# Performance work log

Hardware: AMD Instinct MI355X
Metric: run time of the kernel (lower is better)

## Reference

```python
import jax, jax.numpy as jnp
import numpy as np

N, D = 8192, 768
EPS = 1e-5  # torch LayerNorm default


def setup_inputs() -> dict:
    key = jax.random.key(0)
    ks = jax.random.split(key, 5)
    q = jax.random.normal(ks[0], (N, D), dtype=jnp.float32)
    k = jax.random.normal(ks[1], (N, D), dtype=jnp.float32)
    v = jax.random.normal(ks[2], (N, D), dtype=jnp.float32)
    ln_w = jnp.ones((D,), dtype=jnp.float32)
    ln_b = jnp.zeros((D,), dtype=jnp.float32)
    W_qkv = jax.random.normal(ks[3], (D, D), dtype=jnp.float32) * 0.02
    W_proj = jax.random.normal(ks[4], (D, D), dtype=jnp.float32) * 0.02
    b_proj = jnp.zeros((D,), dtype=jnp.float32)
    return {"q": q, "k": k, "v": v, "ln_w": ln_w, "ln_b": ln_b,
            "W_qkv": W_qkv, "W_proj": W_proj, "b_proj": b_proj}


def reference(q, k, v, ln_w, ln_b, W_qkv, W_proj, b_proj):
    dim = q.shape[-1]
    scale = dim ** (-0.5)

    def ln(x):
        mu = jnp.mean(x, axis=-1, keepdims=True)
        var = jnp.mean((x - mu) ** 2, axis=-1, keepdims=True)
        return (x - mu) * jax.lax.rsqrt(var + EPS) * ln_w + ln_b

    # shared LayerNorm + shared Linear (toto0, no bias) applied to q, k, v
    qn = ln(q) @ W_qkv.T  # [N, D]
    kn = ln(k) @ W_qkv.T
    vn = ln(v) @ W_qkv.T

    attn = jnp.einsum('qc,kc->qk', qn, kn) * scale  # [N, N]
    attn = jax.nn.softmax(attn, axis=-1)
    out = jnp.einsum('qk,kc->qc', attn, vn)  # [N, D]
    out = out @ W_proj.T + b_proj  # proj0
    return out
```

## Files before the change

kernel.cpp:

```cpp
#include <hip/hip_runtime.h>
#include <hip/hip_bf16.h>
#include <stdint.h>

typedef short bf16x8 __attribute__((ext_vector_type(8)));
typedef float f32x4 __attribute__((ext_vector_type(4)));
typedef unsigned short u16;
typedef u16 u16x8 __attribute__((ext_vector_type(8)));

__device__ __forceinline__ u16 f2bf(float x) {
  __hip_bfloat16 h = __float2bfloat16(x);
  return *reinterpret_cast<u16*>(&h);
}
__device__ __forceinline__ float bf2f(u16 v) {
  unsigned u = (unsigned)v << 16;
  return *reinterpret_cast<float*>(&u);
}

__device__ __forceinline__ void gload_lds16(const void* g, const void* lds_base) {
  __builtin_amdgcn_global_load_lds(
      (const __attribute__((address_space(1))) unsigned int*)(uintptr_t)g,
      (__attribute__((address_space(3))) unsigned int*)(uintptr_t)lds_base,
      16, 0, 0);
}

__global__ __launch_bounds__(256) void ln_cast_kernel(
    const float* __restrict__ q, const float* __restrict__ k, const float* __restrict__ v,
    const float* __restrict__ lw, const float* __restrict__ lb, u16* __restrict__ out) {
  int row = blockIdx.x;
  const float* x;
  if (row < 8192) x = q + (size_t)row * 768;
  else if (row < 16384) x = k + (size_t)(row - 8192) * 768;
  else x = v + (size_t)(row - 16384) * 768;
  int t = threadIdx.x;
  float a0 = x[t], a1 = x[t + 256], a2 = x[t + 512];
  __shared__ float red[4];
  __shared__ float red2[4];
  float s = a0 + a1 + a2;
  for (int o = 32; o; o >>= 1) s += __shfl_down(s, o, 64);
  if ((t & 63) == 0) red[t >> 6] = s;
  __syncthreads();
  float mean = (red[0] + red[1] + red[2] + red[3]) * (1.0f / 768.0f);
  float d0 = a0 - mean, d1 = a1 - mean, d2 = a2 - mean;
  float vs = d0 * d0 + d1 * d1 + d2 * d2;
  for (int o = 32; o; o >>= 1) vs += __shfl_down(vs, o, 64);
  if ((t & 63) == 0) red2[t >> 6] = vs;
  __syncthreads();
  float var = (red2[0] + red2[1] + red2[2] + red2[3]) * (1.0f / 768.0f);
  float rstd = rsqrtf(var + 1e-5f);
  u16* o_ = out + (size_t)row * 768;
  o_[t]       = f2bf(d0 * rstd * lw[t]       + lb[t]);
  o_[t + 256] = f2bf(d1 * rstd * lw[t + 256] + lb[t + 256]);
  o_[t + 512] = f2bf(d2 * rstd * lw[t + 512] + lb[t + 512]);
}

__global__ __launch_bounds__(256) void cast_f32_bf16(const float* __restrict__ in,
                                                     u16* __restrict__ out, int n4) {
  int i = blockIdx.x * 256 + threadIdx.x;
  if (i < n4) {
    float4 vv = ((const float4*)in)[i];
    ushort4 o;
    o.x = f2bf(vv.x); o.y = f2bf(vv.y); o.z = f2bf(vv.z); o.w = f2bf(vv.w);
    ((ushort4*)out)[i] = o;
  }
}

__global__ __launch_bounds__(256) void zero_f32(float* __restrict__ p, int n) {
  int i = blockIdx.x * 256 + threadIdx.x;
  if (i < n) p[i] = 0.0f;
}

__global__ __launch_bounds__(256) void transpose64(const u16* __restrict__ in, u16* __restrict__ out) {
  __shared__ __align__(16) u16 tile[64][72];
  int b = blockIdx.x;
  int tr = b / 12, tc = b % 12;
  int t = threadIdx.x;
  int r = t >> 3;
  int cb = (t & 7) << 3;
#pragma unroll
  for (int i = 0; i < 2; i++) {
    int row = r + i * 32;
    const u16* src = in + (size_t)(tr * 64 + row) * 768 + tc * 64 + cb;
    *(uint4*)&tile[row][cb] = *(const uint4*)src;
  }
  __syncthreads();
#pragma unroll
  for (int i = 0; i < 2; i++) {
    int oc = r + i * 32;
    u16x8 tmp;
#pragma unroll
    for (int j = 0; j < 8; j++) tmp[j] = tile[cb + j][oc];
    u16* dst = out + (size_t)(tc * 64 + oc) * 8192 + tr * 64 + cb;
    *(u16x8*)dst = tmp;
  }
}

__global__ __launch_bounds__(256) void reduce4_scale(
    const u16* __restrict__ p0, const u16* __restrict__ p1,
    const u16* __restrict__ p2, const u16* __restrict__ p3,
    const float* __restrict__ rowsum, u16* __restrict__ out, int n8) {
  int i = blockIdx.x * 256 + threadIdx.x;
  if (i < n8) {
    float inv = 1.0f / rowsum[i / 96];
    u16x8 a = ((const u16x8*)p0)[i];
    u16x8 b = ((const u16x8*)p1)[i];
    u16x8 c = ((const u16x8*)p2)[i];
    u16x8 d = ((const u16x8*)p3)[i];
    u16x8 o;
#pragma unroll
    for (int j = 0; j < 8; j++)
      o[j] = f2bf((bf2f(a[j]) + bf2f(b[j]) + bf2f(c[j]) + bf2f(d[j])) * inv);
    ((u16x8*)out)[i] = o;
  }
}

template <int MODE>
__global__ __launch_bounds__(256, 2) void gemm_bt(
    const u16* __restrict__ A0, const u16* __restrict__ B0,
    void* __restrict__ Cv0, void* __restrict__ Cv1,
    int M, int N, int K, int lda, int ldb, int ldc,
    float scale, const float* __restrict__ bias, float* __restrict__ rowsum,
    size_t cSplitStride) {
  __shared__ __align__(16) u16 sA[128 * 64];
  __shared__ __align__(16) u16 sB[128 * 64];
  const int z = blockIdx.y;
  const u16* A = A0 + (size_t)z * (size_t)K;
  const u16* B = B0 + (size_t)z * (size_t)K;
  u16* Cb = (z < 2) ? ((u16*)Cv0 + (size_t)z * cSplitStride)
                    : ((u16*)Cv1 + (size_t)(z - 2) * cSplitStride);
  const int nTn = N >> 7;
  int nwg = gridDim.x, orig = blockIdx.x;
  int qq = nwg >> 3, rr = nwg & 7;
  int xcd = orig & 7, loc = orig >> 3;
  int wg = (xcd < rr ? xcd * (qq + 1) : rr * (qq + 1) + (xcd - rr) * qq) + loc;
  int tm, tn;
  if (nTn == 64 && (M >> 7) == 64) {
    int sb = wg >> 4, in_ = wg & 15;
    tm = ((sb >> 4) << 2) | (in_ >> 2);
    tn = ((sb & 15) << 2) | (in_ & 3);
  } else {
    tm = wg / nTn; tn = wg % nTn;
  }

  const int t = threadIdx.x, l = t & 63, w = t >> 6;
  const int wr = w >> 1, wc = w & 1;
  const int lr = l & 15, kg = (l >> 4) << 3;

  f32x4 acc[4][4];
#pragma unroll
  for (int m = 0; m < 4; m++)
#pragma unroll
    for (int n = 0; n < 4; n++) acc[m][n] = (f32x4){0.f, 0.f, 0.f, 0.f};

  const size_t rowA0 = (size_t)tm * 128;
  const size_t rowB0 = (size_t)tn * 128;
  const int nk = K >> 6;
  for (int kt = 0; kt < nk; kt++) {
    const int k0 = kt << 6;
#pragma unroll
    for (int i = 0; i < 4; i++) {
      int chunk = i * 256 + t;
      int row = chunk >> 3;
      int col = (chunk & 7) << 3;
      gload_lds16(A + (rowA0 + row) * lda + k0 + col, (const char*)sA + (i * 256 + w * 64) * 16);
      gload_lds16(B + (rowB0 + row) * ldb + k0 + col, (const char*)sB + (i * 256 + w * 64) * 16);
    }
    __syncthreads();
#pragma unroll
    for (int kk = 0; kk < 2; kk++) {
      bf16x8 af[4], bfv[4];
#pragma unroll
      for (int m = 0; m < 4; m++)
        af[m] = *(const bf16x8*)&sA[(wr * 64 + m * 16 + lr) * 64 + kk * 32 + kg];
#pragma unroll
      for (int n = 0; n < 4; n++)
        bfv[n] = *(const bf16x8*)&sB[(wc * 64 + n * 16 + lr) * 64 + kk * 32 + kg];
#pragma unroll
      for (int m = 0; m < 4; m++)
#pragma unroll
        for (int n = 0; n < 4; n++)
          acc[m][n] = __builtin_amdgcn_mfma_f32_16x16x32_bf16(af[m], bfv[n], acc[m][n], 0, 0, 0);
    }
    __syncthreads();
  }
  if (MODE == 1) {
    float rs[4][4];
#pragma unroll
    for (int m = 0; m < 4; m++)
#pragma unroll
      for (int j = 0; j < 4; j++) rs[m][j] = 0.0f;
#pragma unroll
    for (int m = 0; m < 4; m++) {
      int rowb = tm * 128 + wr * 64 + m * 16 + ((l >> 4) << 2);
#pragma unroll
      for (int n = 0; n < 4; n++) {
        int col = tn * 128 + wc * 64 + n * 16 + lr;
#pragma unroll
        for (int j = 0; j < 4; j++) {
          float e = __expf(acc[m][n][j] * scale);
          Cb[(size_t)(rowb + j) * ldc + col] = f2bf(e);
          rs[m][j] += e;
        }
      }
    }
#pragma unroll
    for (int m = 0; m < 4; m++) {
      int rowb = tm * 128 + wr * 64 + m * 16 + ((l >> 4) << 2);
#pragma unroll
      for (int j = 0; j < 4; j++) {
        float r = rs[m][j];
        r += __shfl_xor(r, 1);
        r += __shfl_xor(r, 2);
        r += __shfl_xor(r, 4);
        r += __shfl_xor(r, 8);
        if ((l & 15) == 0) atomicAdd(&rowsum[rowb + j], r);
      }
    }
  } else {
#pragma unroll
    for (int m = 0; m < 4; m++) {
      int row = tm * 128 + wr * 64 + m * 16 + ((l >> 4) << 2);
#pragma unroll
      for (int n = 0; n < 4; n++) {
        int col = tn * 128 + wc * 64 + n * 16 + lr;
#pragma unroll
        for (int j = 0; j < 4; j++) {
          float vl = acc[m][n][j];
          if (MODE == 0) Cb[(size_t)(row + j) * ldc + col] = f2bf(vl * scale);
          else ((float*)Cv0)[(size_t)(row + j) * ldc + col] = vl + bias[col];
        }
      }
    }
  }
}

extern "C" void kernel_launch(void* const* d_in, const int* in_sizes, int n_in,
                              void* d_out, int out_size, void* d_ws, size_t ws_size,
                              hipStream_t stream) {
  const float* q  = (const float*)d_in[0];
  const float* k  = (const float*)d_in[1];
  const float* v  = (const float*)d_in[2];
  const float* lw = (const float*)d_in[3];
  const float* lb = (const float*)d_in[4];
  const float* Wq = (const float*)d_in[5];
  const float* Wp = (const float*)d_in[6];
  const float* bp = (const float*)d_in[7];

  char* ws = (char*)d_ws;
  size_t off = 0;
  auto alloc = [&](size_t b) { size_t o = off; off += (b + 255) & ~(size_t)255; return o; };
  size_t o_ln = alloc((size_t)24576 * 768 * 2);
  size_t o_pj = alloc((size_t)24576 * 768 * 2);
  size_t o_wq = alloc((size_t)768 * 768 * 2);
  size_t o_wp = alloc((size_t)768 * 768 * 2);
  u16* lnbuf = (u16*)(ws + o_ln);
  u16* pj    = (u16*)(ws + o_pj);
  u16* wqb   = (u16*)(ws + o_wq);
  u16* wpb   = (u16*)(ws + o_wp);
  const size_t NS = (size_t)8192 * 768;
  u16* vnT = lnbuf;
  u16* p0  = lnbuf + NS;
  u16* p1  = lnbuf + 2 * NS;
  float* rowsum = (float*)(pj + 2 * NS);
  u16* p2 = (u16*)d_out;
  u16* p3 = p2 + NS;
  size_t fixedEnd = off;
  u16* Sbuf = (u16*)(ws + fixedEnd);

  const float scale = 0.03608439182435161f;

  ln_cast_kernel<<<dim3(24576), dim3(256), 0, stream>>>(q, k, v, lw, lb, lnbuf);
  cast_f32_bf16<<<dim3(576), dim3(256), 0, stream>>>(Wq, wqb, 147456);
  cast_f32_bf16<<<dim3(576), dim3(256), 0, stream>>>(Wp, wpb, 147456);

  gemm_bt<0><<<dim3(1152), dim3(256), 0, stream>>>(lnbuf, wqb, (void*)pj, (void*)pj,
      24576, 768, 768, 768, 768, 768, 1.0f, (const float*)nullptr, (float*)nullptr, 0);

  transpose64<<<dim3(1536), dim3(256), 0, stream>>>(pj + (size_t)16384 * 768, vnT);
  zero_f32<<<dim3(32), dim3(256), 0, stream>>>(rowsum, 8192);

  gemm_bt<1><<<dim3(4096), dim3(256), 0, stream>>>(
      pj, pj + NS, (void*)Sbuf, (void*)Sbuf,
      8192, 8192, 768, 768, 768, 8192, scale, (const float*)nullptr, rowsum, 0);

  gemm_bt<0><<<dim3(384, 4), dim3(256), 0, stream>>>(
      Sbuf, vnT, (void*)p0, (void*)p2,
      8192, 768, 2048, 8192, 8192, 768, 1.0f, (const float*)nullptr, (float*)nullptr, NS);

  reduce4_scale<<<dim3(3072), dim3(256), 0, stream>>>(p0, p1, p2, p3, rowsum, p0, (int)(NS / 8));

  gemm_bt<2><<<dim3(384), dim3(256), 0, stream>>>(p0, wpb, d_out, d_out,
      8192, 768, 768, 768, 768, 768, 1.0f, bp, (float*)nullptr, 0);
}
```

Baseline: 381.4 us.

## Add dedicated 256x256 double-buffered QK^T exp kernel with swizzled LDS

```diff
diff --git a/kernel.cpp b/kernel.cpp
--- a/kernel.cpp
+++ b/kernel.cpp
@@ -22,6 +22,10 @@
       (__attribute__((address_space(3))) unsigned int*)(uintptr_t)lds_base,
       16, 0, 0);
 }
+
+#define BAR() __builtin_amdgcn_s_barrier()
+#define LG0() asm volatile("s_waitcnt lgkmcnt(0)" ::: "memory")
+#define VM0() asm volatile("s_waitcnt vmcnt(0)" ::: "memory")
 
 __global__ __launch_bounds__(256) void ln_cast_kernel(
     const float* __restrict__ q, const float* __restrict__ k, const float* __restrict__ v,
@@ -113,13 +117,129 @@
   }
 }
 
+__global__ __launch_bounds__(512, 2) void qk_exp_256(
+    const u16* __restrict__ A, const u16* __restrict__ B, u16* __restrict__ C,
+    float* __restrict__ rowsum, float scale) {
+  __shared__ __align__(16) u16 sA[2][256 * 64];
+  __shared__ __align__(16) u16 sB[2][256 * 64];
+  int orig = blockIdx.x;
+  int wg = (orig & 7) * 128 + (orig >> 3);
+  int tm = wg >> 5, tn = wg & 31;
+  const int t = threadIdx.x, l = t & 63, w = t >> 6;
+  const int wr = w >> 2, wc = w & 3;
+  const int lr = l & 15, lq = l >> 4;
+  const int colb = lq * 16;
+  const int rswz = (lr & 7) << 4;
+
+  f32x4 acc[8][4];
+#pragma unroll
+  for (int m = 0; m < 8; m++)
+#pragma unroll
+    for (int n = 0; n < 4; n++) acc[m][n] = (f32x4){0.f, 0.f, 0.f, 0.f};
+
+  const size_t rA0 = (size_t)tm * 256, rB0 = (size_t)tn * 256;
+
+  auto SCALL = [&](int bufsel, int T, int idx) {
+    const u16* src = (idx < 4) ? A : B;
+    size_t r0 = (idx < 4) ? rA0 : rB0;
+    u16* dstbase = (idx < 4) ? sA[bufsel] : sB[bufsel];
+    int p = idx & 3, k0 = T << 6;
+    int x = p * 8192 + t * 16;
+    int r = x >> 7;
+    int cb = (x & 127) ^ ((r & 7) << 4);
+    gload_lds16((const char*)(src + (r0 + r) * 768 + k0) + cb,
+                (const char*)dstbase + p * 8192 + w * 1024);
+  };
+  auto LOADA = [&](bf16x8 (&aF)[4], int d, int mh, int kk) {
+#pragma unroll
+    for (int mf = 0; mf < 4; mf++) {
+      int arow = wr * 128 + (mh * 4 + mf) * 16 + lr;
+      int x = arow * 128 + kk * 64 + colb;
+      aF[mf] = *(const bf16x8*)((const char*)sA[d] + (x ^ rswz));
+    }
+  };
+  auto LOADB = [&](bf16x8 (&bF)[4], int d, int kk) {
+#pragma unroll
+    for (int nf = 0; nf < 4; nf++) {
+      int brow = wc * 64 + nf * 16 + lr;
+      int x = brow * 128 + kk * 64 + colb;
+      bF[nf] = *(const bf16x8*)((const char*)sB[d] + (x ^ rswz));
+    }
+  };
+  auto MM = [&](bf16x8 (&aF)[4], bf16x8 (&bF)[4], int mh) {
+    __builtin_amdgcn_s_setprio(1);
+#pragma unroll
+    for (int mf = 0; mf < 4; mf++)
+#pragma unroll
+      for (int nf = 0; nf < 4; nf++)
+        acc[mh * 4 + mf][nf] = __builtin_amdgcn_mfma_f32_16x16x32_bf16(
+            aF[mf], bF[nf], acc[mh * 4 + mf][nf], 0, 0, 0);
+    __builtin_amdgcn_s_setprio(0);
+  };
+
+#pragma unroll
+  for (int idx = 0; idx < 8; idx++) SCALL(0, 0, idx);
+  VM0();
+  BAR();
+
+  for (int T = 0; T < 12; T++) {
+    const int cur = T & 1, nxt = cur ^ 1;
+    const bool pf = (T < 11);
+    bf16x8 aF[4], bF0[4], bF1[4];
+    LOADA(aF, cur, 0, 0); LOADB(bF0, cur, 0);
+    if (pf) { SCALL(nxt, T + 1, 0); SCALL(nxt, T + 1, 1); }
+    BAR(); LG0(); MM(aF, bF0, 0); BAR();
+    LOADA(aF, cur, 1, 0);
+    if (pf) { SCALL(nxt, T + 1, 2); SCALL(nxt, T + 1, 3); }
+    BAR(); LG0(); MM(aF, bF0, 1); BAR();
+    LOADA(aF, cur, 0, 1); LOADB(bF1, cur, 1);
+    if (pf) { SCALL(nxt, T + 1, 4); SCALL(nxt, T + 1, 5); }
+    BAR(); LG0(); MM(aF, bF1, 0); BAR();
+    LOADA(aF, cur, 1, 1);
+    if (pf) { SCALL(nxt, T + 1, 6); SCALL(nxt, T + 1, 7); }
+    BAR(); LG0(); MM(aF, bF1, 1);
+    VM0();
+    BAR();
+  }
+
+  float rs[8][4];
+#pragma unroll
+  for (int m = 0; m < 8; m++)
+#pragma unroll
+    for (int j = 0; j < 4; j++) rs[m][j] = 0.0f;
+  const size_t rowBase = rA0 + (size_t)wr * 128;
+  const int colBase = tn * 256 + wc * 64;
+#pragma unroll
+  for (int mi = 0; mi < 8; mi++) {
+    size_t row0 = rowBase + mi * 16 + lq * 4;
+#pragma unroll
+    for (int nf = 0; nf < 4; nf++) {
+      int col = colBase + nf * 16 + lr;
+#pragma unroll
+      for (int j = 0; j < 4; j++) {
+        float e = __expf(acc[mi][nf][j] * scale);
+        C[(row0 + j) * 8192 + col] = f2bf(e);
+        rs[mi][j] += e;
+      }
+    }
+  }
+#pragma unroll
+  for (int mi = 0; mi < 8; mi++)
+#pragma unroll
+    for (int j = 0; j < 4; j++) {
+      float r = rs[mi][j];
+      r += __shfl_xor(r, 1); r += __shfl_xor(r, 2);
+      r += __shfl_xor(r, 4); r += __shfl_xor(r, 8);
+      if (lr == 0) atomicAdd(&rowsum[rowBase + mi * 16 + lq * 4 + j], r);
+    }
+}
+
 template <int MODE>
 __global__ __launch_bounds__(256, 2) void gemm_bt(
     const u16* __restrict__ A0, const u16* __restrict__ B0,
     void* __restrict__ Cv0, void* __restrict__ Cv1,
     int M, int N, int K, int lda, int ldb, int ldc,
-    float scale, const float* __restrict__ bias, float* __restrict__ rowsum,
-    size_t cSplitStride) {
+    float scale, const float* __restrict__ bias, size_t cSplitStride) {
   __shared__ __align__(16) u16 sA[128 * 64];
   __shared__ __align__(16) u16 sB[128 * 64];
   const int z = blockIdx.y;
@@ -132,14 +252,7 @@
   int qq = nwg >> 3, rr = nwg & 7;
   int xcd = orig & 7, loc = orig >> 3;
   int wg = (xcd < rr ? xcd * (qq + 1) : rr * (qq + 1) + (xcd - rr) * qq) + loc;
-  int tm, tn;
-  if (nTn == 64 && (M >> 7) == 64) {
-    int sb = wg >> 4, in_ = wg & 15;
-    tm = ((sb >> 4) << 2) | (in_ >> 2);
-    tn = ((sb & 15) << 2) | (in_ & 3);
-  } else {
-    tm = wg / nTn; tn = wg % nTn;
-  }
+  int tm = wg / nTn, tn = wg % nTn;
 
   const int t = threadIdx.x, l = t & 63, w = t >> 6;
   const int wr = w >> 1, wc = w & 1;
@@ -182,52 +295,17 @@
     }
     __syncthreads();
   }
-  if (MODE == 1) {
-    float rs[4][4];
-#pragma unroll
-    for (int m = 0; m < 4; m++)
-#pragma unroll
-      for (int j = 0; j < 4; j++) rs[m][j] = 0.0f;
-#pragma unroll
-    for (int m = 0; m < 4; m++) {
-      int rowb = tm * 128 + wr * 64 + m * 16 + ((l >> 4) << 2);
-#pragma unroll
-      for (int n = 0; n < 4; n++) {
-        int col = tn * 128 + wc * 64 + n * 16 + lr;
-#pragma unroll
-        for (int j = 0; j < 4; j++) {
-          float e = __expf(acc[m][n][j] * scale);
-          Cb[(size_t)(rowb + j) * ldc + col] = f2bf(e);
-          rs[m][j] += e;
-        }
-      }
-    }
-#pragma unroll
-    for (int m = 0; m < 4; m++) {
-      int rowb = tm * 128 + wr * 64 + m * 16 + ((l >> 4) << 2);
+#pragma unroll
+  for (int m = 0; m < 4; m++) {
+    int row = tm * 128 + wr * 64 + m * 16 + ((l >> 4) << 2);
+#pragma unroll
+    for (int n = 0; n < 4; n++) {
+      int col = tn * 128 + wc * 64 + n * 16 + lr;
 #pragma unroll
       for (int j = 0; j < 4; j++) {
-        float r = rs[m][j];
-        r += __shfl_xor(r, 1);
-        r += __shfl_xor(r, 2);
-        r += __shfl_xor(r, 4);
-        r += __shfl_xor(r, 8);
-        if ((l & 15) == 0) atomicAdd(&rowsum[rowb + j], r);
-      }
-    }
-  } else {
-#pragma unroll
-    for (int m = 0; m < 4; m++) {
-      int row = tm * 128 + wr * 64 + m * 16 + ((l >> 4) << 2);
-#pragma unroll
-      for (int n = 0; n < 4; n++) {
-        int col = tn * 128 + wc * 64 + n * 16 + lr;
-#pragma unroll
-        for (int j = 0; j < 4; j++) {
-          float vl = acc[m][n][j];
-          if (MODE == 0) Cb[(size_t)(row + j) * ldc + col] = f2bf(vl * scale);
-          else ((float*)Cv0)[(size_t)(row + j) * ldc + col] = vl + bias[col];
-        }
+        float vl = acc[m][n][j];
+        if (MODE == 0) Cb[(size_t)(row + j) * ldc + col] = f2bf(vl * scale);
+        else ((float*)Cv0)[(size_t)(row + j) * ldc + col] = vl + bias[col];
       }
     }
   }
@@ -273,21 +351,19 @@
   cast_f32_bf16<<<dim3(576), dim3(256), 0, stream>>>(Wp, wpb, 147456);
 
   gemm_bt<0><<<dim3(1152), dim3(256), 0, stream>>>(lnbuf, wqb, (void*)pj, (void*)pj,
-      24576, 768, 768, 768, 768, 768, 1.0f, (const float*)nullptr, (float*)nullptr, 0);
+      24576, 768, 768, 768, 768, 768, 1.0f, (const float*)nullptr, 0);
 
   transpose64<<<dim3(1536), dim3(256), 0, stream>>>(pj + (size_t)16384 * 768, vnT);
   zero_f32<<<dim3(32), dim3(256), 0, stream>>>(rowsum, 8192);
 
-  gemm_bt<1><<<dim3(4096), dim3(256), 0, stream>>>(
-      pj, pj + NS, (void*)Sbuf, (void*)Sbuf,
-      8192, 8192, 768, 768, 768, 8192, scale, (const float*)nullptr, rowsum, 0);
+  qk_exp_256<<<dim3(1024), dim3(512), 0, stream>>>(pj, pj + NS, Sbuf, rowsum, scale);
 
   gemm_bt<0><<<dim3(384, 4), dim3(256), 0, stream>>>(
       Sbuf, vnT, (void*)p0, (void*)p2,
-      8192, 768, 2048, 8192, 8192, 768, 1.0f, (const float*)nullptr, (float*)nullptr, NS);
+      8192, 768, 2048, 8192, 8192, 768, 1.0f, (const float*)nullptr, NS);
 
   reduce4_scale<<<dim3(3072), dim3(256), 0, stream>>>(p0, p1, p2, p3, rowsum, p0, (int)(NS / 8));
 
   gemm_bt<2><<<dim3(384), dim3(256), 0, stream>>>(p0, wpb, d_out, d_out,
-      8192, 768, 768, 768, 768, 768, 1.0f, bp, (float*)nullptr, 0);
-}
+      8192, 768, 768, 768, 768, 768, 1.0f, bp, 0);
+}
```

New measurement: 398.4 us. +4.5%, slower.
